# Kernel optimization log

Hardware: AMD Instinct MI355X
Metric: run time of the kernel (lower is better)

## Reference

```python
import math
import jax, jax.numpy as jnp
import numpy as np

B, T, C, H, V = 2, 512, 768, 12, 50304
HD = C // H
EPS_LN = 1e-5
SINK_ITERS = 6           # MAX_ITER_SINK
N_STEPS = 20             # ceil((1-0)/h_max), h_max=0.05
H_STEP = 1.0 / N_STEPS   # Euler step size h


def layer_norm(x, w, b):
    mu = jnp.mean(x, axis=-1, keepdims=True)
    var = jnp.mean(jnp.square(x - mu), axis=-1, keepdims=True)
    return (x - mu) * jax.lax.rsqrt(var + EPS_LN) * w + b


def sinkhorn_pi(Cmat):
    # log-domain Sinkhorn (eps=1) on cost matrix Cmat [N, T, T]; returns transport plan pi
    n = Cmat.shape[-1]
    log_marg = -jnp.log(jnp.asarray(n, Cmat.dtype))  # log(1/n), uniform marginals
    u = jnp.zeros(Cmat.shape[:-1], Cmat.dtype)
    v = jnp.zeros(Cmat.shape[:-1], Cmat.dtype)
    def M(u, v):
        return -Cmat + u[..., :, None] + v[..., None, :]
    for _ in range(SINK_ITERS):
        u = (log_marg - jax.nn.logsumexp(M(u, v), axis=-1)) + u
        v = (log_marg - jax.nn.logsumexp(M(u, v), axis=-2)) + v
    return jnp.exp(M(u, v))


def block_f(z, t, attn_ln_w, attn_ln_b, c_attn_w, c_attn_b, c_proj_w, c_proj_b,
            mlp_ln_w, mlp_ln_b, c_fc_w, c_fc_b, mlp_proj_w, mlp_proj_b):
    Bz, Tz, Cz = z.shape
    tcol = jnp.full((Bz, Tz, 1), t, z.dtype)
    # attention sub-block: LN over C+1 dims (x concat time)
    x = layer_norm(jnp.concatenate([z, tcol], axis=-1), attn_ln_w, attn_ln_b)
    qkv = x @ c_attn_w + c_attn_b                      # [B,T,3C]
    q, k, v = jnp.split(qkv, 3, axis=-1)
    q = q.reshape(Bz, Tz, H, HD).transpose(0, 2, 1, 3)  # [B,H,T,hd]
    k = k.reshape(Bz, Tz, H, HD).transpose(0, 2, 1, 3)
    v = v.reshape(Bz, Tz, H, HD).transpose(0, 2, 1, 3)
    att = jnp.einsum('bhqd,bhkd->bhqk', q, k) * (1.0 / math.sqrt(HD))
    mask = jnp.tril(jnp.ones((Tz, Tz), dtype=bool))
    att = jax.nn.softmax(jnp.where(mask, att, -jnp.inf), axis=-1)
    pi = sinkhorn_pi(att.reshape(Bz * H, Tz, Tz)) * Tz  # sink(att)[0] * n
    y = jnp.einsum('bhqk,bhkd->bhqd', pi.reshape(Bz, H, Tz, Tz), v)
    y = y.transpose(0, 2, 1, 3).reshape(Bz, Tz, Cz)
    y = y @ c_proj_w + c_proj_b
    # MLP sub-block on LN(concat(attn_out, t))
    ht = layer_norm(jnp.concatenate([y, tcol], axis=-1), mlp_ln_w, mlp_ln_b)
    h1 = jax.nn.gelu(ht @ c_fc_w + c_fc_b, approximate=False)
    return h1 @ mlp_proj_w + mlp_proj_b


def setup_inputs() -> dict:
    key = jax.random.key(0)
    ks = jax.random.split(key, 8)
    s = 0.02
    return {
        'idx': jax.random.randint(ks[0], (B, T), 0, V),
        'wte': s * jax.random.normal(ks[1], (V, C), jnp.float32),
        'wpe': s * jax.random.normal(ks[2], (T, C), jnp.float32),
        'attn_ln_w': jnp.ones((C + 1,), jnp.float32),
        'attn_ln_b': jnp.zeros((C + 1,), jnp.float32),
        'c_attn_w': s * jax.random.normal(ks[3], (C + 1, 3 * C), jnp.float32),
        'c_attn_b': jnp.zeros((3 * C,), jnp.float32),
        'c_proj_w': s * jax.random.normal(ks[4], (C, C), jnp.float32),
        'c_proj_b': jnp.zeros((C,), jnp.float32),
        'mlp_ln_w': jnp.ones((C + 1,), jnp.float32),
        'mlp_ln_b': jnp.zeros((C + 1,), jnp.float32),
        'c_fc_w': s * jax.random.normal(ks[5], (C + 1, 4 * C), jnp.float32),
        'c_fc_b': jnp.zeros((4 * C,), jnp.float32),
        'mlp_proj_w': s * jax.random.normal(ks[6], (4 * C, C), jnp.float32),
        'mlp_proj_b': jnp.zeros((C,), jnp.float32),
        'lnf_w': jnp.ones((C,), jnp.float32),
        'lnf_b': jnp.zeros((C,), jnp.float32),
    }


def reference(idx, wte, wpe, attn_ln_w, attn_ln_b, c_attn_w, c_attn_b, c_proj_w,
              c_proj_b, mlp_ln_w, mlp_ln_b, c_fc_w, c_fc_b, mlp_proj_w, mlp_proj_b,
              lnf_w, lnf_b):
    x = wte[idx] + wpe[jnp.arange(idx.shape[1])]  # [B,T,C]

    def step(carry, _):
        z, t = carry
        dz = block_f(z, t, attn_ln_w, attn_ln_b, c_attn_w, c_attn_b, c_proj_w,
                     c_proj_b, mlp_ln_w, mlp_ln_b, c_fc_w, c_fc_b, mlp_proj_w,
                     mlp_proj_b)
        return (z + H_STEP * dz, t + H_STEP), None

    (x, _), _ = jax.lax.scan(step, (x, jnp.float32(0.0)), None, length=N_STEPS)
    x = layer_norm(x, lnf_w, lnf_b)
    logits = x[:, -1:, :] @ wte.T  # inference path: last position only, tied head
    return logits
```

## Files before the change

### kernel.cpp

```cpp
#include <hip/hip_runtime.h>
#include <hip/hip_bf16.h>
#include <math.h>

typedef unsigned short ushortT;
typedef unsigned int uintT;

#define Bc   2
#define Tc   512
#define Cc   768
#define Hc   12
#define HDc  64
#define Vc   50304
#define BTc  (Bc*Tc)
#define NHc  (Bc*Hc)
#define C3   (3*Cc)
#define C4   (4*Cc)
#define EPS_LN 1e-5f
#define H_STEP 0.05f
#define INVN (1.0f/512.0f)
#define SB   4
#define ELP  (Tc + 8)

typedef float f32x4 __attribute__((ext_vector_type(4)));
typedef __bf16 bf16x8 __attribute__((ext_vector_type(8)));
typedef ushortT us8 __attribute__((ext_vector_type(8)));
typedef uintT u32x4 __attribute__((ext_vector_type(4)));

__device__ __forceinline__ ushortT f2bf(float f) {
    union { float f; unsigned u; } x; x.f = f;
    unsigned r = (x.u + 0x7fffu + ((x.u >> 16) & 1u)) >> 16;
    return (ushortT)r;
}
__device__ __forceinline__ float bf2f(ushortT b) {
    union { unsigned u; float f; } x; x.u = ((unsigned)b) << 16;
    return x.f;
}
__device__ __forceinline__ float bflo(uintT w) {
    union { unsigned u; float f; } x; x.u = w << 16;
    return x.f;
}
__device__ __forceinline__ float bfhi(uintT w) {
    union { unsigned u; float f; } x; x.u = w & 0xffff0000u;
    return x.f;
}

__device__ __forceinline__ void gll16(const ushortT* g, ushortT* l) {
    __builtin_amdgcn_global_load_lds(
        (const __attribute__((address_space(1))) unsigned int*)g,
        (__attribute__((address_space(3))) unsigned int*)l,
        16, 0, 0);
}

__device__ __forceinline__ float waveReduceSumX(float v) {
    for (int o = 32; o; o >>= 1) v += __shfl_xor(v, o);
    return v;
}
__device__ __forceinline__ float blockReduceSum(float v) {
    __shared__ float sm[4];
    for (int o = 32; o; o >>= 1) v += __shfl_down(v, o);
    __syncthreads();
    if ((threadIdx.x & 63) == 0) sm[threadIdx.x >> 6] = v;
    __syncthreads();
    return sm[0] + sm[1] + sm[2] + sm[3];
}

__global__ __launch_bounds__(256)
void wtrans_kernel(const float* __restrict__ W, ushortT* __restrict__ out,
                   int K, int N)
{
    __shared__ float t[32][33];
    int k0 = blockIdx.x * 32, n0 = blockIdx.y * 32;
    int tx = threadIdx.x & 31, ty = threadIdx.x >> 5;
    for (int r = ty; r < 32; r += 8)
        t[r][tx] = W[(size_t)(k0 + r) * N + n0 + tx];
    __syncthreads();
    for (int r = ty; r < 32; r += 8)
        out[(size_t)(n0 + r) * K + k0 + tx] = f2bf(t[tx][r]);
}

__global__ __launch_bounds__(256)
void embed_ln(const int* __restrict__ idx, const float* __restrict__ wte,
              const float* __restrict__ wpe, float* __restrict__ z,
              const float* __restrict__ lnw, const float* __restrict__ lnb,
              ushortT* __restrict__ xlnb, float* __restrict__ xt)
{
    int row = blockIdx.x, tid = threadIdx.x;
    int tok = idx[row];
    float v[3];
#pragma unroll
    for (int q = 0; q < 3; ++q) {
        int c = tid + 256 * q;
        float val = wte[(size_t)tok * Cc + c] + wpe[(size_t)(row & (Tc - 1)) * Cc + c];
        z[(size_t)row * Cc + c] = val;
        v[q] = val;
    }
    float s = blockReduceSum(v[0] + v[1] + v[2]);
    float mu = s / 769.f;
    float d0 = v[0] - mu, d1 = v[1] - mu, d2 = v[2] - mu;
    float ss = blockReduceSum(d0 * d0 + d1 * d1 + d2 * d2);
    float dt = 0.f - mu;
    float var = (ss + dt * dt) / 769.f;
    float rs = rsqrtf(var + EPS_LN);
#pragma unroll
    for (int q = 0; q < 3; ++q) {
        int c = tid + 256 * q;
        xlnb[(size_t)row * Cc + c] = f2bf((v[q] - mu) * rs * lnw[c] + lnb[c]);
    }
    if (tid == 0) xt[row] = dt * rs * lnw[Cc] + lnb[Cc];
}

__global__ __launch_bounds__(256)
void ln_kernel(const float* __restrict__ X, const float* __restrict__ w,
               const float* __restrict__ bb, void* __restrict__ Y,
               float* __restrict__ yt, int hasT, float tval,
               int rowMul, int rowAdd, int obf16)
{
    int orow = blockIdx.x;
    int r = orow * rowMul + rowAdd;
    const float* x = X + (size_t)r * Cc;
    int tid = threadIdx.x;
    float xv[3];
#pragma unroll
    for (int q = 0; q < 3; ++q) xv[q] = x[tid + 256 * q];
    float s = blockReduceSum(xv[0] + xv[1] + xv[2]);
    float cnt = hasT ? 769.f : 768.f;
    float mu = (s + (hasT ? tval : 0.f)) / cnt;
    float d0 = xv[0] - mu, d1 = xv[1] - mu, d2 = xv[2] - mu;
    float ss = blockReduceSum(d0 * d0 + d1 * d1 + d2 * d2);
    float dt = tval - mu;
    float var = (ss + (hasT ? dt * dt : 0.f)) / cnt;
    float rs = rsqrtf(var + EPS_LN);
#pragma unroll
    for (int q = 0; q < 3; ++q) {
        int c = tid + 256 * q;
        float v = (xv[q] - mu) * rs * w[c] + bb[c];
        if (obf16) ((ushortT*)Y)[(size_t)orow * Cc + c] = f2bf(v);
        else       ((float*)Y)[(size_t)orow * Cc + c] = v;
    }
    if (hasT && tid == 0) yt[orow] = dt * rs * w[Cc] + bb[Cc];
}

template <int EPI>
__global__ __launch_bounds__(256)
void gemm_bt(const ushortT* __restrict__ A, int lda,
             const ushortT* __restrict__ Bt, int ldb,
             void* __restrict__ Cm, int ldc, int K,
             const float* __restrict__ bias,
             const float* __restrict__ extraA,
             const float* __restrict__ extraB)
{
    __shared__ __align__(16) ushortT Als[128][32];
    __shared__ __align__(16) ushortT Bls[128][32];
    if (EPI == 4) {
        int koff = blockIdx.z * K;
        A += koff; Bt += koff;
    }
    int tid = threadIdx.x;
    int lane = tid & 63, wid = tid >> 6;
    int wm = wid >> 1, wn = wid & 1;
    int m0 = blockIdx.y * 128, n0 = blockIdx.x * 128;
    f32x4 acc[4][4];
    const f32x4 fz = {0.f, 0.f, 0.f, 0.f};
#pragma unroll
    for (int i = 0; i < 4; ++i)
#pragma unroll
        for (int j = 0; j < 4; ++j) acc[i][j] = fz;

    for (int k0 = 0; k0 < K; k0 += 32) {
#pragma unroll
        for (int is = 0; is < 2; ++is) {
            int ch = is * 256 + tid;
            int m = ch >> 2, kc = ch & 3;
            gll16(A + (size_t)(m0 + m) * lda + k0 + kc * 8, &Als[0][0] + ch * 8);
            gll16(Bt + (size_t)(n0 + m) * ldb + k0 + kc * 8, &Bls[0][0] + ch * 8);
        }
        __syncthreads();
        bf16x8 af[4], bfv[4];
#pragma unroll
        for (int i = 0; i < 4; ++i) {
            int row = wm * 64 + i * 16 + (lane & 15);
            af[i] = *(const bf16x8*)&Als[row][(lane >> 4) * 8];
            int col = wn * 64 + i * 16 + (lane & 15);
            bfv[i] = *(const bf16x8*)&Bls[col][(lane >> 4) * 8];
        }
#pragma unroll
        for (int i = 0; i < 4; ++i)
#pragma unroll
            for (int j = 0; j < 4; ++j)
                acc[i][j] = __builtin_amdgcn_mfma_f32_16x16x32_bf16(af[i], bfv[j], acc[i][j], 0, 0, 0);
        __syncthreads();
    }
#pragma unroll
    for (int i = 0; i < 4; ++i) {
#pragma unroll
        for (int j = 0; j < 4; ++j) {
#pragma unroll
            for (int r = 0; r < 4; ++r) {
                int row = m0 + wm * 64 + i * 16 + (lane >> 4) * 4 + r;
                int col = n0 + wn * 64 + j * 16 + (lane & 15);
                float v = acc[i][j][r];
                if (extraA) v += extraA[row] * extraB[col];
                if (bias) v += bias[col];
                size_t oi = (size_t)row * ldc + col;
                if (EPI == 0) {
                    ((ushortT*)Cm)[oi] = f2bf(v);
                } else if (EPI == 1) {
                    v = 0.5f * v * (1.f + erff(v * 0.70710678118654752440f));
                    ((ushortT*)Cm)[oi] = f2bf(v);
                } else if (EPI == 3) {
                    ((float*)Cm)[oi] = v;
                } else if (EPI == 4) {
                    ((float*)Cm)[(size_t)blockIdx.z * ((size_t)BTc * Cc) + oi] = v;
                }
            }
        }
    }
}

__global__ __launch_bounds__(512)
void sinkfused(const ushortT* __restrict__ qkvb, ushortT* __restrict__ y,
               float* __restrict__ partials, unsigned* __restrict__ ctr,
               unsigned barBase)
{
    int gb = blockIdx.x;
    int n = gb >> 2, r = gb & 3;
    int row0 = r * 128;
    int b = n / Hc, h = n - b * Hc;
    int tid = threadIdx.x;
    int l = tid & 63, w = tid >> 6;
    __shared__ __align__(16) ushortT Els[128][ELP];
    __shared__ __align__(16) ushortT Kshare[128 * 64];
    __shared__ float a_s[128];
    __shared__ float b_s[Tc];
    const f32x4 fz = {0.f, 0.f, 0.f, 0.f};

    int qrow = b * Tc + row0 + w * 16 + (l & 15);
    const ushortT* qp = qkvb + (size_t)qrow * C3 + h * HDc + (l >> 4) * 8;
    bf16x8 aq0 = *(const bf16x8*)(qp);
    bf16x8 aq1 = *(const bf16x8*)(qp + 32);

    int kcmax = r + 1;
    f32x4 acc[32];
#pragma unroll
    for (int j = 0; j < 32; ++j) acc[j] = fz;

#pragma unroll
    for (int kc = 0; kc < 4; ++kc) {
        if (kc < kcmax) {
            {
                int ch = tid;
                int row = ch >> 3, c16 = (ch & 7) ^ (row & 7);
                gll16(qkvb + (size_t)(b * Tc + kc * 128 + row) * C3 + Cc + h * HDc + c16 * 8,
                      Kshare + ch * 8);
                ch = tid + 512;
                row = ch >> 3; c16 = (ch & 7) ^ (row & 7);
                gll16(qkvb + (size_t)(b * Tc + kc * 128 + row) * C3 + Cc + h * HDc + c16 * 8,
                      Kshare + ch * 8);
            }
            __syncthreads();
#pragma unroll
            for (int jj = 0; jj < 8; ++jj) {
                int krow = jj * 16 + (l & 15);
                int c16a = (l >> 4);
                int c16b = 4 + (l >> 4);
                bf16x8 bk0 = *(const bf16x8*)(Kshare + ((size_t)krow * 8 + (c16a ^ (krow & 7))) * 8);
                bf16x8 bk1 = *(const bf16x8*)(Kshare + ((size_t)krow * 8 + (c16b ^ (krow & 7))) * 8);
                acc[kc * 8 + jj] = __builtin_amdgcn_mfma_f32_16x16x32_bf16(aq0, bk0, acc[kc * 8 + jj], 0, 0, 0);
                acc[kc * 8 + jj] = __builtin_amdgcn_mfma_f32_16x16x32_bf16(aq1, bk1, acc[kc * 8 + jj], 0, 0, 0);
            }
            __syncthreads();
        }
    }

    int nvalid = kcmax * 8;
    int colbase = (l & 15);
    int rowa[4];
#pragma unroll
    for (int e = 0; e < 4; ++e) rowa[e] = row0 + w * 16 + (l >> 4) * 4 + e;

    float mx[4] = {-INFINITY, -INFINITY, -INFINITY, -INFINITY};
#pragma unroll
    for (int j = 0; j < 32; ++j) {
        if (j < nvalid) {
            int col = j * 16 + colbase;
#pragma unroll
            for (int e = 0; e < 4; ++e)
                if (col <= rowa[e]) mx[e] = fmaxf(mx[e], acc[j][e] * 0.125f);
        }
    }
#pragma unroll
    for (int e = 0; e < 4; ++e)
        for (int o = 1; o < 16; o <<= 1) mx[e] = fmaxf(mx[e], __shfl_xor(mx[e], o));

    float se[4] = {0.f, 0.f, 0.f, 0.f};
#pragma unroll
    for (int j = 0; j < 32; ++j) {
        if (j < nvalid) {
            int col = j * 16 + colbase;
#pragma unroll
            for (int e = 0; e < 4; ++e) {
                float exv = (col <= rowa[e]) ? __expf(acc[j][e] * 0.125f - mx[e]) : 0.f;
                acc[j][e] = exv;
                se[e] += exv;
            }
        }
    }
#pragma unroll
    for (int e = 0; e < 4; ++e)
        for (int o = 1; o < 16; o <<= 1) se[e] += __shfl_xor(se[e], o);
    float inv[4];
#pragma unroll
    for (int e = 0; e < 4; ++e) inv[e] = 1.f / se[e];

    float rsum[4] = {0.f, 0.f, 0.f, 0.f};
#pragma unroll
    for (int j = 0; j < 32; ++j) {
        if (j < nvalid) {
            int col = j * 16 + colbase;
#pragma unroll
            for (int e = 0; e < 4; ++e) {
                float Ee = __expf(-(acc[j][e] * inv[e]));
                rsum[e] += Ee;
                Els[w * 16 + (l >> 4) * 4 + e][col] = f2bf(Ee);
            }
        }
    }
#pragma unroll
    for (int e = 0; e < 4; ++e) {
        for (int o = 1; o < 16; o <<= 1) rsum[e] += __shfl_xor(rsum[e], o);
        if ((l & 15) == 0)
            a_s[w * 16 + (l >> 4) * 4 + e] = INVN / (rsum[e] + (float)(Tc - nvalid * 16));
    }
    {
        int tailc = 64 - kcmax * 16;
        if (tailc > 0) {
            us8 ones8;
#pragma unroll
            for (int e = 0; e < 8; ++e) ones8[e] = 0x3F80;
            for (int idx2 = l; idx2 < 16 * tailc; idx2 += 64) {
                int rr = idx2 / tailc, cc = idx2 - rr * tailc;
                *(us8*)&Els[w * 16 + rr][(kcmax * 16 + cc) * 8] = ones8;
            }
        }
    }
    __syncthreads();

    float* mypart = partials + (size_t)(n * SB + r) * Tc;
    const float* hpart = partials + (size_t)n * SB * Tc;
    unsigned* myctr = ctr + n * 16;
    float* scr = (float*)Kshare;

#pragma unroll 1
    for (int p = 0; p < 11; ++p) {
        if ((p & 1) == 0) {
            int cg = tid & 63, sl = tid >> 6;
            float ac[8] = {0.f, 0.f, 0.f, 0.f, 0.f, 0.f, 0.f, 0.f};
#pragma unroll
            for (int i = 0; i < 16; ++i) {
                int row = sl * 16 + i;
                us8 ev = *(const us8*)&Els[row][cg * 8];
                float fa = a_s[row];
#pragma unroll
                for (int e = 0; e < 8; ++e)
                    ac[e] += bf2f(ev[e]) * fa;
            }
            f32x4 lo = {ac[0], ac[1], ac[2], ac[3]};
            f32x4 hi = {ac[4], ac[5], ac[6], ac[7]};
            *(f32x4*)&scr[sl * 512 + cg * 8] = lo;
            *(f32x4*)&scr[sl * 512 + cg * 8 + 4] = hi;
            __syncthreads();
            int j = tid;
            float accs = 0.f;
#pragma unroll
            for (int s2 = 0; s2 < 8; ++s2) accs += scr[s2 * 512 + j];
            __hip_atomic_store(&mypart[j], accs, __ATOMIC_RELAXED, __HIP_MEMORY_SCOPE_AGENT);
            __syncthreads();
            if (tid == 0) {
                __threadfence();
                atomicAdd(myctr, 1u);
                unsigned tgt = barBase + (unsigned)(p / 2 + 1) * SB;
                while (__hip_atomic_load(myctr, __ATOMIC_ACQUIRE, __HIP_MEMORY_SCOPE_AGENT) < tgt)
                    __builtin_amdgcn_s_sleep(2);
            }
            __syncthreads();
            float s0 = __hip_atomic_load(&hpart[j], __ATOMIC_RELAXED, __HIP_MEMORY_SCOPE_AGENT);
            float s1 = __hip_atomic_load(&hpart[Tc + j], __ATOMIC_RELAXED, __HIP_MEMORY_SCOPE_AGENT);
            float s2 = __hip_atomic_load(&hpart[2 * Tc + j], __ATOMIC_RELAXED, __HIP_MEMORY_SCOPE_AGENT);
            float s3 = __hip_atomic_load(&hpart[3 * Tc + j], __ATOMIC_RELAXED, __HIP_MEMORY_SCOPE_AGENT);
            b_s[j] = INVN / (s0 + s1 + s2 + s3);
            __syncthreads();
        } else {
            f32x4 b0 = *(const f32x4*)&b_s[l * 8];
            f32x4 b1 = *(const f32x4*)&b_s[l * 8 + 4];
            float breg[8] = {b0[0], b0[1], b0[2], b0[3], b1[0], b1[1], b1[2], b1[3]};
#pragma unroll 1
            for (int k = 0; k < 16; k += 4) {
                int r0 = w * 16 + k;
                u32x4 q0 = *(const u32x4*)(&Els[r0 + 0][l * 8]);
                u32x4 q1 = *(const u32x4*)(&Els[r0 + 1][l * 8]);
                u32x4 q2 = *(const u32x4*)(&Els[r0 + 2][l * 8]);
                u32x4 q3 = *(const u32x4*)(&Els[r0 + 3][l * 8]);
                float s0 = 0.f, s1 = 0.f, s2 = 0.f, s3 = 0.f;
#pragma unroll
                for (int c = 0; c < 4; ++c) {
                    s0 += bflo(q0[c]) * breg[2 * c] + bfhi(q0[c]) * breg[2 * c + 1];
                    s1 += bflo(q1[c]) * breg[2 * c] + bfhi(q1[c]) * breg[2 * c + 1];
                    s2 += bflo(q2[c]) * breg[2 * c] + bfhi(q2[c]) * breg[2 * c + 1];
                    s3 += bflo(q3[c]) * breg[2 * c] + bfhi(q3[c]) * breg[2 * c + 1];
                }
                s0 = waveReduceSumX(s0);
                s1 = waveReduceSumX(s1);
                s2 = waveReduceSumX(s2);
                s3 = waveReduceSumX(s3);
                if (l == 0) {
                    a_s[r0 + 0] = INVN / s0;
                    a_s[r0 + 1] = INVN / s1;
                    a_s[r0 + 2] = INVN / s2;
                    a_s[r0 + 3] = INVN / s3;
                }
            }
            __syncthreads();
        }
    }

    {
        ushortT* Kls2 = Kshare;
        int wm = w >> 1, wn = w & 1;
        f32x4 acc2[2][2];
#pragma unroll
        for (int i = 0; i < 2; ++i)
#pragma unroll
            for (int j = 0; j < 2; ++j) acc2[i][j] = fz;
        const ushortT* vbase = qkvb + (size_t)(b * Tc) * C3 + 2 * Cc + h * HDc;

#pragma unroll 1
        for (int k0 = 0; k0 < Tc; k0 += 64) {
            {
                int tt = tid >> 3, dblk = tid & 7;
                us8 vv = *(const us8*)(vbase + (size_t)(k0 + tt) * C3 + dblk * 8);
                float bs = 512.f * b_s[k0 + tt];
#pragma unroll
                for (int e = 0; e < 8; ++e)
                    Kls2[(dblk * 8 + e) * 72 + tt] = f2bf(bf2f(vv[e]) * bs);
            }
            __syncthreads();
#pragma unroll
            for (int kk = 0; kk < 64; kk += 32) {
                bf16x8 af[2], bv[2];
#pragma unroll
                for (int i = 0; i < 2; ++i)
                    af[i] = *(const bf16x8*)&Els[wm * 32 + i * 16 + (l & 15)][k0 + kk + (l >> 4) * 8];
#pragma unroll
                for (int j = 0; j < 2; ++j)
                    bv[j] = *(const bf16x8*)(Kls2 + (size_t)(wn * 32 + j * 16 + (l & 15)) * 72 + kk + (l >> 4) * 8);
#pragma unroll
                for (int i = 0; i < 2; ++i)
#pragma unroll
                    for (int j = 0; j < 2; ++j)
                        acc2[i][j] = __builtin_amdgcn_mfma_f32_16x16x32_bf16(af[i], bv[j], acc2[i][j], 0, 0, 0);
            }
            __syncthreads();
        }
#pragma unroll
        for (int i = 0; i < 2; ++i)
#pragma unroll
            for (int j = 0; j < 2; ++j)
#pragma unroll
                for (int rr = 0; rr < 4; ++rr) {
                    int lrow = wm * 32 + i * 16 + (l >> 4) * 4 + rr;
                    float a_r = a_s[lrow];
                    int grow = b * Tc + row0 + lrow;
                    int gcol = h * HDc + wn * 32 + j * 16 + (l & 15);
                    y[(size_t)grow * Cc + gcol] = f2bf(acc2[i][j][rr] * a_r);
                }
    }
}

__global__ __launch_bounds__(256)
void reduce_ln(const float* __restrict__ parts, const float* __restrict__ bias,
               float* __restrict__ z, const float* __restrict__ lnw,
               const float* __restrict__ lnb, ushortT* __restrict__ xlnb,
               float* __restrict__ xt, float tval)
{
    int row = blockIdx.x, tid = threadIdx.x;
    const size_t CS = (size_t)BTc * Cc;
    float v[3];
#pragma unroll
    for (int q = 0; q < 3; ++q) {
        int c = tid + 256 * q;
        size_t idx = (size_t)row * Cc + c;
        float s = parts[idx] + parts[CS + idx] + parts[2 * CS + idx]
                + parts[3 * CS + idx] + bias[c];
        v[q] = z[idx] + H_STEP * s;
        z[idx] = v[q];
    }
    float s = blockReduceSum(v[0] + v[1] + v[2]);
    float mu = (s + tval) / 769.f;
    float d0 = v[0] - mu, d1 = v[1] - mu, d2 = v[2] - mu;
    float ss = blockReduceSum(d0 * d0 + d1 * d1 + d2 * d2);
    float dt = tval - mu;
    float var = (ss + dt * dt) / 769.f;
    float rs = rsqrtf(var + EPS_LN);
#pragma unroll
    for (int q = 0; q < 3; ++q) {
        int c = tid + 256 * q;
        xlnb[(size_t)row * Cc + c] = f2bf((v[q] - mu) * rs * lnw[c] + lnb[c]);
    }
    if (tid == 0) xt[row] = dt * rs * lnw[Cc] + lnb[Cc];
}

__global__ __launch_bounds__(256)
void logits_kernel(const float* __restrict__ xf, const float* __restrict__ wte,
                   float* __restrict__ out)
{
    __shared__ __align__(16) float xs[2 * Cc];
    int tid = threadIdx.x;
    for (int i = tid; i < 384; i += 256)
        ((f32x4*)xs)[i] = ((const f32x4*)xf)[i];
    __syncthreads();
    int w = tid >> 6, lane = tid & 63;
    int vrow = blockIdx.x * 4 + w;
    const f32x4* wr = (const f32x4*)(wte + (size_t)vrow * Cc);
    const f32x4* x0 = (const f32x4*)xs;
    const f32x4* x1 = (const f32x4*)(xs + Cc);
    float a0 = 0.f, a1 = 0.f;
#pragma unroll
    for (int it = 0; it < 3; ++it) {
        int k4 = it * 64 + lane;
        f32x4 wv = wr[k4];
        f32x4 p = x0[k4], q = x1[k4];
        a0 += wv[0] * p[0] + wv[1] * p[1] + wv[2] * p[2] + wv[3] * p[3];
        a1 += wv[0] * q[0] + wv[1] * q[1] + wv[2] * q[2] + wv[3] * q[3];
    }
    for (int o = 32; o; o >>= 1) {
        a0 += __shfl_down(a0, o);
        a1 += __shfl_down(a1, o);
    }
    if (lane == 0) {
        out[vrow] = a0;
        out[Vc + vrow] = a1;
    }
}

extern "C" void kernel_launch(void* const* d_in, const int* in_sizes, int n_in,
                              void* d_out, int out_size, void* d_ws, size_t ws_size,
                              hipStream_t stream)
{
    const int*   idx        = (const int*)  d_in[0];
    const float* wte        = (const float*)d_in[1];
    const float* wpe        = (const float*)d_in[2];
    const float* attn_ln_w  = (const float*)d_in[3];
    const float* attn_ln_b  = (const float*)d_in[4];
    const float* c_attn_w   = (const float*)d_in[5];
    const float* c_attn_b   = (const float*)d_in[6];
    const float* c_proj_w   = (const float*)d_in[7];
    const float* c_proj_b   = (const float*)d_in[8];
    const float* mlp_ln_w   = (const float*)d_in[9];
    const float* mlp_ln_b   = (const float*)d_in[10];
    const float* c_fc_w     = (const float*)d_in[11];
    const float* c_fc_b     = (const float*)d_in[12];
    const float* mlp_proj_w = (const float*)d_in[13];
    const float* mlp_proj_b = (const float*)d_in[14];
    const float* lnf_w      = (const float*)d_in[15];
    const float* lnf_b      = (const float*)d_in[16];
    float* out = (float*)d_out;

    char* base = (char*)d_ws;
    size_t off = 0;
    auto alloc = [&](size_t bytes) -> void* {
        void* p = base + off;
        off = (off + bytes + 255) & ~(size_t)255;
        return p;
    };
    float*   z     = (float*)  alloc((size_t)BTc * Cc * 4);
    float*   parts = (float*)  alloc((size_t)4 * BTc * Cc * 4);
    ushortT* qkvb  = (ushortT*)alloc((size_t)BTc * C3 * 2);
    ushortT* xlnb  = (ushortT*)alloc((size_t)BTc * Cc * 2);
    ushortT* y     = (ushortT*)alloc((size_t)BTc * Cc * 2);
    ushortT* h1    = (ushortT*)alloc((size_t)BTc * C4 * 2);
    float*   ao    = (float*)  alloc((size_t)BTc * Cc * 4);
    float*   xt    = (float*)  alloc(BTc * 4);
    float*   partv = (float*)  alloc((size_t)NHc * SB * Tc * 4);
    unsigned* ctr  = (unsigned*)alloc(NHc * 16 * 4);
    float*   xf    = (float*)  alloc(2 * Cc * 4);
    ushortT* WqkvT = (ushortT*)alloc((size_t)C3 * Cc * 2);
    ushortT* WprojT= (ushortT*)alloc((size_t)Cc * Cc * 2);
    ushortT* WfcT  = (ushortT*)alloc((size_t)C4 * Cc * 2);
    ushortT* WmlpT = (ushortT*)alloc((size_t)Cc * C4 * 2);

    hipMemsetAsync(ctr, 0, NHc * 16 * 4, stream);
    embed_ln<<<BTc, 256, 0, stream>>>(idx, wte, wpe, z, attn_ln_w, attn_ln_b, xlnb, xt);
    wtrans_kernel<<<dim3(Cc / 32, C3 / 32), 256, 0, stream>>>(c_attn_w,   WqkvT,  Cc, C3);
    wtrans_kernel<<<dim3(Cc / 32, Cc / 32), 256, 0, stream>>>(c_proj_w,   WprojT, Cc, Cc);
    wtrans_kernel<<<dim3(Cc / 32, C4 / 32), 256, 0, stream>>>(c_fc_w,     WfcT,   Cc, C4);
    wtrans_kernel<<<dim3(C4 / 32, Cc / 32), 256, 0, stream>>>(mlp_proj_w, WmlpT,  C4, Cc);

    float t = 0.f;
    for (int step = 0; step < 20; ++step) {
        gemm_bt<0><<<dim3(C3 / 128, BTc / 128), 256, 0, stream>>>(
            xlnb, Cc, WqkvT, Cc, qkvb, C3, Cc,
            c_attn_b, xt, c_attn_w + (size_t)Cc * C3);
        sinkfused<<<NHc * SB, 512, 0, stream>>>(
            qkvb, y, partv, ctr, (unsigned)(step * 6 * SB));
        gemm_bt<3><<<dim3(Cc / 128, BTc / 128), 256, 0, stream>>>(
            y, Cc, WprojT, Cc, ao, Cc, Cc,
            c_proj_b, nullptr, nullptr);
        ln_kernel<<<BTc, 256, 0, stream>>>(ao, mlp_ln_w, mlp_ln_b, xlnb, xt, 1, t, 1, 0, 1);
        gemm_bt<1><<<dim3(C4 / 128, BTc / 128), 256, 0, stream>>>(
            xlnb, Cc, WfcT, Cc, h1, C4, Cc,
            c_fc_b, xt, c_fc_w + (size_t)Cc * C4);
        gemm_bt<4><<<dim3(Cc / 128, BTc / 128, 4), 256, 0, stream>>>(
            h1, C4, WmlpT, C4, parts, Cc, C4 / 4,
            nullptr, nullptr, nullptr);
        t += H_STEP;
        reduce_ln<<<BTc, 256, 0, stream>>>(parts, mlp_proj_b, z,
                                           attn_ln_w, attn_ln_b, xlnb, xt, t);
    }

    ln_kernel<<<2, 256, 0, stream>>>(z, lnf_w, lnf_b, xf, nullptr, 0, 0.f, Tc, Tc - 1, 0);
    logits_kernel<<<Vc / 4, 256, 0, stream>>>(xf, wte, out);
}
```

Before: 4.020 ms.

## Drop split-K MLP projection; fuse residual update into GEMM epilogue, bf16 attn output

```diff
diff --git a/kernel.cpp b/kernel.cpp
--- a/kernel.cpp
+++ b/kernel.cpp
@@ -110,18 +110,24 @@
 }
 
 __global__ __launch_bounds__(256)
-void ln_kernel(const float* __restrict__ X, const float* __restrict__ w,
+void ln_kernel(const void* __restrict__ X, const float* __restrict__ w,
                const float* __restrict__ bb, void* __restrict__ Y,
                float* __restrict__ yt, int hasT, float tval,
-               int rowMul, int rowAdd, int obf16)
+               int rowMul, int rowAdd, int obf16, int ibf16)
 {
     int orow = blockIdx.x;
     int r = orow * rowMul + rowAdd;
-    const float* x = X + (size_t)r * Cc;
     int tid = threadIdx.x;
     float xv[3];
-#pragma unroll
-    for (int q = 0; q < 3; ++q) xv[q] = x[tid + 256 * q];
+    if (ibf16) {
+        const ushortT* x = (const ushortT*)X + (size_t)r * Cc;
+#pragma unroll
+        for (int q = 0; q < 3; ++q) xv[q] = bf2f(x[tid + 256 * q]);
+    } else {
+        const float* x = (const float*)X + (size_t)r * Cc;
+#pragma unroll
+        for (int q = 0; q < 3; ++q) xv[q] = x[tid + 256 * q];
+    }
     float s = blockReduceSum(xv[0] + xv[1] + xv[2]);
     float cnt = hasT ? 769.f : 768.f;
     float mu = (s + (hasT ? tval : 0.f)) / cnt;
@@ -151,10 +157,6 @@
 {
     __shared__ __align__(16) ushortT Als[128][32];
     __shared__ __align__(16) ushortT Bls[128][32];
-    if (EPI == 4) {
-        int koff = blockIdx.z * K;
-        A += koff; Bt += koff;
-    }
     int tid = threadIdx.x;
     int lane = tid & 63, wid = tid >> 6;
     int wm = wid >> 1, wn = wid & 1;
@@ -207,10 +209,9 @@
                 } else if (EPI == 1) {
                     v = 0.5f * v * (1.f + erff(v * 0.70710678118654752440f));
                     ((ushortT*)Cm)[oi] = f2bf(v);
-                } else if (EPI == 3) {
-                    ((float*)Cm)[oi] = v;
-                } else if (EPI == 4) {
-                    ((float*)Cm)[(size_t)blockIdx.z * ((size_t)BTc * Cc) + oi] = v;
+                } else if (EPI == 2) {
+                    float* Z = (float*)Cm;
+                    Z[oi] = Z[oi] + H_STEP * v;
                 }
             }
         }
@@ -223,7 +224,7 @@
                unsigned barBase)
 {
     int gb = blockIdx.x;
-    int n = gb >> 2, r = gb & 3;
+    int n = gb % NHc, r = gb / NHc;
     int row0 = r * 128;
     int b = n / Hc, h = n - b * Hc;
     int tid = threadIdx.x;
@@ -474,39 +475,6 @@
                     y[(size_t)grow * Cc + gcol] = f2bf(acc2[i][j][rr] * a_r);
                 }
     }
-}
-
-__global__ __launch_bounds__(256)
-void reduce_ln(const float* __restrict__ parts, const float* __restrict__ bias,
-               float* __restrict__ z, const float* __restrict__ lnw,
-               const float* __restrict__ lnb, ushortT* __restrict__ xlnb,
-               float* __restrict__ xt, float tval)
-{
-    int row = blockIdx.x, tid = threadIdx.x;
-    const size_t CS = (size_t)BTc * Cc;
-    float v[3];
-#pragma unroll
-    for (int q = 0; q < 3; ++q) {
-        int c = tid + 256 * q;
-        size_t idx = (size_t)row * Cc + c;
-        float s = parts[idx] + parts[CS + idx] + parts[2 * CS + idx]
-                + parts[3 * CS + idx] + bias[c];
-        v[q] = z[idx] + H_STEP * s;
-        z[idx] = v[q];
-    }
-    float s = blockReduceSum(v[0] + v[1] + v[2]);
-    float mu = (s + tval) / 769.f;
-    float d0 = v[0] - mu, d1 = v[1] - mu, d2 = v[2] - mu;
-    float ss = blockReduceSum(d0 * d0 + d1 * d1 + d2 * d2);
-    float dt = tval - mu;
-    float var = (ss + dt * dt) / 769.f;
-    float rs = rsqrtf(var + EPS_LN);
-#pragma unroll
-    for (int q = 0; q < 3; ++q) {
-        int c = tid + 256 * q;
-        xlnb[(size_t)row * Cc + c] = f2bf((v[q] - mu) * rs * lnw[c] + lnb[c]);
-    }
-    if (tid == 0) xt[row] = dt * rs * lnw[Cc] + lnb[Cc];
 }
 
 __global__ __launch_bounds__(256)
@@ -573,12 +541,11 @@
         return p;
     };
     float*   z     = (float*)  alloc((size_t)BTc * Cc * 4);
-    float*   parts = (float*)  alloc((size_t)4 * BTc * Cc * 4);
     ushortT* qkvb  = (ushortT*)alloc((size_t)BTc * C3 * 2);
     ushortT* xlnb  = (ushortT*)alloc((size_t)BTc * Cc * 2);
     ushortT* y     = (ushortT*)alloc((size_t)BTc * Cc * 2);
     ushortT* h1    = (ushortT*)alloc((size_t)BTc * C4 * 2);
-    float*   ao    = (float*)  alloc((size_t)BTc * Cc * 4);
+    ushortT* aob   = (ushortT*)alloc((size_t)BTc * Cc * 2);
     float*   xt    = (float*)  alloc(BTc * 4);
     float*   partv = (float*)  alloc((size_t)NHc * SB * Tc * 4);
     unsigned* ctr  = (unsigned*)alloc(NHc * 16 * 4);
@@ -602,21 +569,20 @@
             c_attn_b, xt, c_attn_w + (size_t)Cc * C3);
         sinkfused<<<NHc * SB, 512, 0, stream>>>(
             qkvb, y, partv, ctr, (unsigned)(step * 6 * SB));
-        gemm_bt<3><<<dim3(Cc / 128, BTc / 128), 256, 0, stream>>>(
-            y, Cc, WprojT, Cc, ao, Cc, Cc,
+        gemm_bt<0><<<dim3(Cc / 128, BTc / 128), 256, 0, stream>>>(
+            y, Cc, WprojT, Cc, aob, Cc, Cc,
             c_proj_b, nullptr, nullptr);
-        ln_kernel<<<BTc, 256, 0, stream>>>(ao, mlp_ln_w, mlp_ln_b, xlnb, xt, 1, t, 1, 0, 1);
+        ln_kernel<<<BTc, 256, 0, stream>>>(aob, mlp_ln_w, mlp_ln_b, xlnb, xt, 1, t, 1, 0, 1, 1);
         gemm_bt<1><<<dim3(C4 / 128, BTc / 128), 256, 0, stream>>>(
             xlnb, Cc, WfcT, Cc, h1, C4, Cc,
             c_fc_b, xt, c_fc_w + (size_t)Cc * C4);
-        gemm_bt<4><<<dim3(Cc / 128, BTc / 128, 4), 256, 0, stream>>>(
-            h1, C4, WmlpT, C4, parts, Cc, C4 / 4,
-            nullptr, nullptr, nullptr);
+        gemm_bt<2><<<dim3(Cc / 128, BTc / 128), 256, 0, stream>>>(
+            h1, C4, WmlpT, C4, z, Cc, C4,
+            mlp_proj_b, nullptr, nullptr);
         t += H_STEP;
-        reduce_ln<<<BTc, 256, 0, stream>>>(parts, mlp_proj_b, z,
-                                           attn_ln_w, attn_ln_b, xlnb, xt, t);
-    }
-
-    ln_kernel<<<2, 256, 0, stream>>>(z, lnf_w, lnf_b, xf, nullptr, 0, 0.f, Tc, Tc - 1, 0);
+        ln_kernel<<<BTc, 256, 0, stream>>>(z, attn_ln_w, attn_ln_b, xlnb, xt, 1, t, 1, 0, 1, 0);
+    }
+
+    ln_kernel<<<2, 256, 0, stream>>>(z, lnf_w, lnf_b, xf, nullptr, 0, 0.f, Tc, Tc - 1, 0, 0);
     logits_kernel<<<Vc / 4, 256, 0, stream>>>(xf, wte, out);
 }
```

Measured after the change: 5.403 ms. 1.34x slower.
